# Performance work log

Measured on AMD Instinct MI355X. Metric: run time of the kernel, lower is better.

The kernel has to match this reference:

```python
import jax, jax.numpy as jnp
import numpy as np

HIDDEN = 4096
NUM_HEADS = 32
NUM_KV_HEADS = 8
HEAD_DIM = 128


def setup_inputs() -> dict:
    key = jax.random.key(0)
    k0, k1, k2, k3, k4 = jax.random.split(key, 5)
    B, S = 1, 2048
    s = 0.02
    return {
        "hidden_states": jax.random.normal(k0, (B, S, HIDDEN), dtype=jnp.float32),
        "Wq": jax.random.normal(k1, (HIDDEN, NUM_HEADS * HEAD_DIM), dtype=jnp.float32) * s,
        "Wk": jax.random.normal(k2, (HIDDEN, NUM_KV_HEADS * HEAD_DIM), dtype=jnp.float32) * s,
        "Wv": jax.random.normal(k3, (HIDDEN, NUM_KV_HEADS * HEAD_DIM), dtype=jnp.float32) * s,
        "Wo": jax.random.normal(k4, (NUM_HEADS * HEAD_DIM, HIDDEN), dtype=jnp.float32) * s,
    }


def reference(hidden_states, Wq, Wk, Wv, Wo):
    B, S, _ = hidden_states.shape
    n_rep = NUM_HEADS // NUM_KV_HEADS
    # Projections -> [B, H, S, D]
    q = (hidden_states @ Wq).reshape(B, S, NUM_HEADS, HEAD_DIM).transpose(0, 2, 1, 3)
    k = (hidden_states @ Wk).reshape(B, S, NUM_KV_HEADS, HEAD_DIM).transpose(0, 2, 1, 3)
    v = (hidden_states @ Wv).reshape(B, S, NUM_KV_HEADS, HEAD_DIM).transpose(0, 2, 1, 3)
    # GQA expansion: repeat_interleave KV heads to match query head count
    k = jnp.repeat(k, n_rep, axis=1)
    v = jnp.repeat(v, n_rep, axis=1)
    scale = HEAD_DIM ** -0.5
    # Full [B, H, S, S] attention scores (faithful to the naive reference)
    scores = jnp.einsum("bhqd,bhkd->bhqk", q, k) * scale
    causal = jnp.tril(jnp.ones((S, S), dtype=bool))
    scores = jnp.where(causal[None, None], scores, jnp.float32(-jnp.inf))
    probs = jax.nn.softmax(scores, axis=-1)
    out = jnp.einsum("bhqk,bhkd->bhqd", probs, v)
    out = out.transpose(0, 2, 1, 3).reshape(B, S, NUM_HEADS * HEAD_DIM)
    return out @ Wo
```

## Files before the change

kernel.cpp:

```cpp
#include <hip/hip_runtime.h>
#include <hip/hip_bf16.h>

typedef __bf16 bf16;
typedef __bf16 bf16x4 __attribute__((ext_vector_type(4)));
typedef __bf16 bf16x8 __attribute__((ext_vector_type(8)));
typedef float  f32x4  __attribute__((ext_vector_type(4)));

#define SEQ  2048
#define HID  4096
#define QKVN 6144

__device__ __forceinline__ void gload_lds16(const void* g, void* l) {
  __builtin_amdgcn_global_load_lds(
      (const __attribute__((address_space(1))) void*)g,
      (__attribute__((address_space(3))) void*)l, 16, 0, 0);
}

__global__ __launch_bounds__(256) void cast_f32_bf16(const float* __restrict__ in,
                                                     bf16* __restrict__ out, int n) {
  int i = (blockIdx.x * 256 + threadIdx.x) * 4;
  int stride = gridDim.x * 256 * 4;
  for (; i < n; i += stride) {
    float4 v = *(const float4*)(in + i);
    bf16x4 o;
    o[0] = (bf16)v.x; o[1] = (bf16)v.y; o[2] = (bf16)v.z; o[3] = (bf16)v.w;
    *(bf16x4*)(out + i) = o;
  }
}

__global__ __launch_bounds__(256) void transpose_cast(const float* __restrict__ W,
                                                      bf16* __restrict__ Wt,
                                                      int N, int roff) {
  __shared__ float tile[32][33];
  int k0 = blockIdx.y * 32;
  int n0 = blockIdx.x * 32;
  int t = threadIdx.x;
  int r = t >> 5, c = t & 31;
#pragma unroll
  for (int p = 0; p < 4; ++p)
    tile[r + p * 8][c] = W[(size_t)(k0 + r + p * 8) * N + n0 + c];
  __syncthreads();
#pragma unroll
  for (int p = 0; p < 4; ++p)
    Wt[(size_t)(roff + n0 + r + p * 8) * 4096 + k0 + c] = (bf16)tile[c][r + p * 8];
}

__global__ __launch_bounds__(256) void transpose_v(const bf16* __restrict__ QKV,
                                                   bf16* __restrict__ Vt_g) {
  __shared__ bf16 tile[32][33];
  int s0 = blockIdx.x * 32;
  int d0 = blockIdx.y * 32;
  int g  = blockIdx.z;
  int t = threadIdx.x;
  int r = t >> 5, c = t & 31;
#pragma unroll
  for (int p = 0; p < 4; ++p)
    tile[r + p * 8][c] = QKV[(size_t)(s0 + r + p * 8) * QKVN + 5120 + g * 128 + d0 + c];
  __syncthreads();
#pragma unroll
  for (int p = 0; p < 4; ++p)
    Vt_g[(size_t)(g * 128 + d0 + r + p * 8) * SEQ + s0 + c] = tile[c][r + p * 8];
}

template <typename OUT_T>
__global__ __launch_bounds__(256) void gemm_bt(const bf16* __restrict__ A,
                                               const bf16* __restrict__ Bt,
                                               OUT_T* __restrict__ C,
                                               int K, int ldc) {
  __shared__ __align__(16) bf16 Abuf[128 * 32];
  __shared__ __align__(16) bf16 Bbuf[128 * 32];
  int m0 = blockIdx.y * 128, n0 = blockIdx.x * 128;
  int tid = threadIdx.x, w = tid >> 6, lane = tid & 63;
  int wr = w >> 1, wc = w & 1;
  int l15 = lane & 15, l4 = lane >> 4;
  f32x4 acc[4][4] = {};
  const int nk = K >> 5;
  for (int kt = 0; kt < nk; ++kt) {
    int k0 = kt << 5;
#pragma unroll
    for (int p = 0; p < 2; ++p) {
      int elem = p * 2048 + w * 512 + lane * 8;
      int row = elem >> 5, col = elem & 31;
      gload_lds16(A + (size_t)(m0 + row) * K + k0 + col, (char*)Abuf + 2 * elem);
      gload_lds16(Bt + (size_t)(n0 + row) * K + k0 + col, (char*)Bbuf + 2 * elem);
    }
    __syncthreads();
    bf16x8 af[4], bfr[4];
#pragma unroll
    for (int m = 0; m < 4; ++m)
      af[m] = *(const bf16x8*)(Abuf + (wr * 64 + m * 16 + l15) * 32 + l4 * 8);
#pragma unroll
    for (int n = 0; n < 4; ++n)
      bfr[n] = *(const bf16x8*)(Bbuf + (wc * 64 + n * 16 + l15) * 32 + l4 * 8);
#pragma unroll
    for (int m = 0; m < 4; ++m)
#pragma unroll
      for (int n = 0; n < 4; ++n)
        acc[m][n] = __builtin_amdgcn_mfma_f32_16x16x32_bf16(af[m], bfr[n], acc[m][n], 0, 0, 0);
    __syncthreads();
  }
#pragma unroll
  for (int m = 0; m < 4; ++m)
#pragma unroll
    for (int n = 0; n < 4; ++n)
#pragma unroll
      for (int i = 0; i < 4; ++i) {
        int row = m0 + wr * 64 + m * 16 + l4 * 4 + i;
        int col = n0 + wc * 64 + n * 16 + l15;
        C[(size_t)row * ldc + col] = (OUT_T)acc[m][n][i];
      }
}

__global__ __launch_bounds__(512, 2) void attn_kernel(const bf16* __restrict__ QKV,
                                                      const bf16* __restrict__ Vt_g,
                                                      bf16* __restrict__ attn) {
  __shared__ __align__(16) bf16 Klds[2][64 * 128];
  __shared__ __align__(16) bf16 Vlds[2][64 * 128];
  __shared__ __align__(16) bf16 Plds[8 * 16 * 64];
  const int bid = blockIdx.x;
  const int g = bid & 7;
  const int rest = bid >> 3;
  const int hg = rest & 1;
  const int pair = rest >> 1;
  const int qb_a = pair, qb_b = 31 - pair;
  const int tid = threadIdx.x, w = tid >> 6, lane = tid & 63;
  const int hsel = w >> 2, qw = w & 3;
  const int h = g * 4 + hg * 2 + hsel;
  const int l15 = lane & 15, l4 = lane >> 4;
  const int wqA = qb_a * 64 + qw * 16;
  const int wqB = qb_b * 64 + qw * 16;
  const int qcol = h * 128;
  const int kcol = 4096 + g * 128;
  const float scale = 0.08838834764831845f;
  const float LOG2E = 1.4426950408889634f;

  const bf16* Vhead = Vt_g + (size_t)g * 128 * SEQ;

  bf16x8 aqA[4], aqB[4];
#pragma unroll
  for (int kc = 0; kc < 4; ++kc) {
    aqA[kc] = *(const bf16x8*)(QKV + (size_t)(wqA + l15) * QKVN + qcol + kc * 32 + l4 * 8);
    aqB[kc] = *(const bf16x8*)(QKV + (size_t)(wqB + l15) * QKVN + qcol + kc * 32 + l4 * 8);
  }

  f32x4 acc_oA[8] = {}, acc_oB[8] = {};
  float mA[4], lA[4], mB[4], lB[4];
#pragma unroll
  for (int i = 0; i < 4; ++i) { mA[i] = -1e30f; lA[i] = 0.f; mB[i] = -1e30f; lB[i] = 0.f; }

  auto stageKV = [&](int kb, int buf) {
#pragma unroll
    for (int j = 0; j < 2; ++j) {
      int c = tid + (j << 9);
      int krow = c >> 4, kslot = c & 15;
      gload_lds16((const char*)(QKV + (size_t)(kb + krow) * QKVN + kcol) +
                      ((kslot ^ (krow & 7)) << 4),
                  (char*)Klds[buf] + c * 16);
      int vrow = c >> 3, vslot = c & 7;
      gload_lds16(Vhead + (size_t)vrow * SEQ + kb + ((vslot ^ (vrow & 7)) << 3),
                  (char*)Vlds[buf] + c * 16);
    }
  };

  auto compute_block = [&](const bf16x8* aq, f32x4* acc_o, float* mrow, float* lrow,
                           int wq0, int kb, int cur) {
    const char* Kbuf = (const char*)Klds[cur];
    const char* Vbuf = (const char*)Vlds[cur];
    f32x4 accs[4] = {};
#pragma unroll
    for (int n = 0; n < 4; ++n) {
      int row_ = n * 16 + l15;
      int sw = (row_ & 7) << 4;
#pragma unroll
      for (int kc = 0; kc < 4; ++kc) {
        bf16x8 bk = *(const bf16x8*)(Kbuf + row_ * 256 + ((kc * 64 + l4 * 16) ^ sw));
        accs[n] = __builtin_amdgcn_mfma_f32_16x16x32_bf16(aq[kc], bk, accs[n], 0, 0, 0);
      }
    }
    bool needmask = (kb + 64 > wq0);
    float s[4][4];
#pragma unroll
    for (int n = 0; n < 4; ++n)
#pragma unroll
      for (int i = 0; i < 4; ++i) {
        float v = accs[n][i] * scale;
        if (needmask) {
          int ks = kb + n * 16 + l15;
          int qr = wq0 + l4 * 4 + i;
          if (ks > qr) v = -1e30f;
        }
        s[n][i] = v;
      }
    float fac[4], ps[4][4];
#pragma unroll
    for (int i = 0; i < 4; ++i) {
      float t = fmaxf(fmaxf(s[0][i], s[1][i]), fmaxf(s[2][i], s[3][i]));
      t = fmaxf(t, __shfl_xor(t, 1));
      t = fmaxf(t, __shfl_xor(t, 2));
      t = fmaxf(t, __shfl_xor(t, 4));
      t = fmaxf(t, __shfl_xor(t, 8));
      float mnew = fmaxf(mrow[i], t);
      fac[i] = exp2f((mrow[i] - mnew) * LOG2E);
      float psum = 0.f;
#pragma unroll
      for (int n = 0; n < 4; ++n) {
        float p = exp2f((s[n][i] - mnew) * LOG2E);
        ps[n][i] = p; psum += p;
      }
      psum += __shfl_xor(psum, 1);
      psum += __shfl_xor(psum, 2);
      psum += __shfl_xor(psum, 4);
      psum += __shfl_xor(psum, 8);
      lrow[i] = lrow[i] * fac[i] + psum;
      mrow[i] = mnew;
    }
#pragma unroll
    for (int n2 = 0; n2 < 8; ++n2)
#pragma unroll
      for (int i = 0; i < 4; ++i)
        acc_o[n2][i] *= fac[i];
    char* Pw = (char*)Plds + w * 2048;
#pragma unroll
    for (int n = 0; n < 4; ++n)
#pragma unroll
      for (int i = 0; i < 4; ++i) {
        int r = l4 * 4 + i;
        int b = (r * 128 + (n * 16 + l15) * 2) ^ ((r & 7) << 4);
        *(bf16*)(Pw + b) = (bf16)ps[n][i];
      }
    __builtin_amdgcn_sched_barrier(0);
    asm volatile("" ::: "memory");
    bf16x8 pa[2];
#pragma unroll
    for (int kc = 0; kc < 2; ++kc)
      pa[kc] = *(const bf16x8*)(Pw + (l15 * 128 + ((kc * 64 + l4 * 16) ^ ((l15 & 7) << 4))));
#pragma unroll
    for (int n2 = 0; n2 < 8; ++n2) {
      int row_ = n2 * 16 + l15;
      int sw = (row_ & 7) << 4;
#pragma unroll
      for (int kc = 0; kc < 2; ++kc) {
        bf16x8 bv = *(const bf16x8*)(Vbuf + row_ * 128 + ((kc * 64 + l4 * 16) ^ sw));
        acc_o[n2] = __builtin_amdgcn_mfma_f32_16x16x32_bf16(pa[kc], bv, acc_o[n2], 0, 0, 0);
      }
    }
    asm volatile("" ::: "memory");
  };

  stageKV(0, 0);
  __syncthreads();

  int cur = 0;
  for (int kbi = 0; kbi <= qb_b; ++kbi) {
    int kb = kbi * 64;
    if (kbi < qb_b) stageKV(kb + 64, cur ^ 1);
    if (kbi <= qb_a) compute_block(aqA, acc_oA, mA, lA, wqA, kb, cur);
    compute_block(aqB, acc_oB, mB, lB, wqB, kb, cur);
    __syncthreads();
    cur ^= 1;
  }

#pragma unroll
  for (int n2 = 0; n2 < 8; ++n2)
#pragma unroll
    for (int i = 0; i < 4; ++i) {
      int col = qcol + n2 * 16 + l15;
      attn[(size_t)(wqA + l4 * 4 + i) * 4096 + col] = (bf16)(acc_oA[n2][i] / lA[i]);
      attn[(size_t)(wqB + l4 * 4 + i) * 4096 + col] = (bf16)(acc_oB[n2][i] / lB[i]);
    }
}

extern "C" void kernel_launch(void* const* d_in, const int* in_sizes, int n_in,
                              void* d_out, int out_size, void* d_ws, size_t ws_size,
                              hipStream_t stream) {
  const float* X  = (const float*)d_in[0];
  const float* Wq = (const float*)d_in[1];
  const float* Wk = (const float*)d_in[2];
  const float* Wv = (const float*)d_in[3];
  const float* Wo = (const float*)d_in[4];
  float* out = (float*)d_out;

  const size_t XB_OFF  = 0;
  const size_t WT_OFF  = 16777216;
  const size_t VT_OFF  = WT_OFF + 33554432;
  const size_t QKV_OFF = 16777216 + 50331648;
  if (ws_size < (size_t)92274688) return;

  char* ws = (char*)d_ws;
  bf16* Xb    = (bf16*)(ws + XB_OFF);
  bf16* Wt    = (bf16*)(ws + WT_OFF);
  bf16* Vt_g  = (bf16*)(ws + VT_OFF);
  bf16* QKV   = (bf16*)(ws + QKV_OFF);
  bf16* attnb = Xb;

  cast_f32_bf16<<<2048, 256, 0, stream>>>(X, Xb, SEQ * HID);
  transpose_cast<<<dim3(4096 / 32, 4096 / 32), 256, 0, stream>>>(Wq, Wt, 4096, 0);
  transpose_cast<<<dim3(1024 / 32, 4096 / 32), 256, 0, stream>>>(Wk, Wt, 1024, 4096);
  transpose_cast<<<dim3(1024 / 32, 4096 / 32), 256, 0, stream>>>(Wv, Wt, 1024, 5120);
  gemm_bt<bf16><<<dim3(QKVN / 128, SEQ / 128), 256, 0, stream>>>(Xb, Wt, QKV, HID, QKVN);
  transpose_cast<<<dim3(4096 / 32, 4096 / 32), 256, 0, stream>>>(Wo, Wt, 4096, 0);
  transpose_v<<<dim3(SEQ / 32, 4, 8), 256, 0, stream>>>(QKV, Vt_g);
  attn_kernel<<<256, 512, 0, stream>>>(QKV, Vt_g, attnb);
  gemm_bt<float><<<dim3(4096 / 128, SEQ / 128), 256, 0, stream>>>(attnb, Wt, out, HID, 4096);
}
```

Before: 413.9 us.

## Deepen GEMM K-tile with swizzled LDS, add lazy softmax rescale and MFMA priority

The GEMM K-tile per iteration grows from 32 to 64, using an XOR-swizzled LDS layout to avoid bank conflicts and halving the number of barriers per K. The attention kernel skips the online-softmax rescale of the accumulators unless some row's max has grown by more than a threshold, following the FA4 lazy-rescale trick. It also raises wave priority around the MFMA sections with s_setprio. Lazy rescaling lets probabilities exceed 1 (up to about e^8) before normalization, which is fine in fp32 but relies on the bf16 P values staying in range. The larger tiles double GEMM LDS use.

```diff
diff --git a/kernel.cpp b/kernel.cpp
--- a/kernel.cpp
+++ b/kernel.cpp
@@ -67,36 +67,50 @@
                                                const bf16* __restrict__ Bt,
                                                OUT_T* __restrict__ C,
                                                int K, int ldc) {
-  __shared__ __align__(16) bf16 Abuf[128 * 32];
-  __shared__ __align__(16) bf16 Bbuf[128 * 32];
+  __shared__ __align__(16) bf16 Abuf[128 * 64];
+  __shared__ __align__(16) bf16 Bbuf[128 * 64];
   int m0 = blockIdx.y * 128, n0 = blockIdx.x * 128;
   int tid = threadIdx.x, w = tid >> 6, lane = tid & 63;
   int wr = w >> 1, wc = w & 1;
   int l15 = lane & 15, l4 = lane >> 4;
   f32x4 acc[4][4] = {};
-  const int nk = K >> 5;
+  const int nk = K >> 6;
   for (int kt = 0; kt < nk; ++kt) {
-    int k0 = kt << 5;
-#pragma unroll
-    for (int p = 0; p < 2; ++p) {
-      int elem = p * 2048 + w * 512 + lane * 8;
-      int row = elem >> 5, col = elem & 31;
-      gload_lds16(A + (size_t)(m0 + row) * K + k0 + col, (char*)Abuf + 2 * elem);
-      gload_lds16(Bt + (size_t)(n0 + row) * K + k0 + col, (char*)Bbuf + 2 * elem);
+    int k0 = kt << 6;
+#pragma unroll
+    for (int p = 0; p < 4; ++p) {
+      int c = p * 256 + tid;
+      int row = c >> 3, slot = c & 7;
+      int ssl = (slot ^ (row & 7)) << 4;
+      gload_lds16((const char*)(A + (size_t)(m0 + row) * K + k0) + ssl, (char*)Abuf + c * 16);
+      gload_lds16((const char*)(Bt + (size_t)(n0 + row) * K + k0) + ssl, (char*)Bbuf + c * 16);
     }
     __syncthreads();
-    bf16x8 af[4], bfr[4];
+    bf16x8 af[4][2], bfr[4][2];
 #pragma unroll
     for (int m = 0; m < 4; ++m)
-      af[m] = *(const bf16x8*)(Abuf + (wr * 64 + m * 16 + l15) * 32 + l4 * 8);
+#pragma unroll
+      for (int kk = 0; kk < 2; ++kk) {
+        int row = wr * 64 + m * 16 + l15;
+        af[m][kk] = *(const bf16x8*)((const char*)Abuf + row * 128 +
+                                     (((kk * 4 + l4) ^ (row & 7)) << 4));
+      }
 #pragma unroll
     for (int n = 0; n < 4; ++n)
-      bfr[n] = *(const bf16x8*)(Bbuf + (wc * 64 + n * 16 + l15) * 32 + l4 * 8);
-#pragma unroll
-    for (int m = 0; m < 4; ++m)
-#pragma unroll
-      for (int n = 0; n < 4; ++n)
-        acc[m][n] = __builtin_amdgcn_mfma_f32_16x16x32_bf16(af[m], bfr[n], acc[m][n], 0, 0, 0);
+#pragma unroll
+      for (int kk = 0; kk < 2; ++kk) {
+        int row = wc * 64 + n * 16 + l15;
+        bfr[n][kk] = *(const bf16x8*)((const char*)Bbuf + row * 128 +
+                                      (((kk * 4 + l4) ^ (row & 7)) << 4));
+      }
+#pragma unroll
+    for (int kk = 0; kk < 2; ++kk)
+#pragma unroll
+      for (int m = 0; m < 4; ++m)
+#pragma unroll
+        for (int n = 0; n < 4; ++n)
+          acc[m][n] = __builtin_amdgcn_mfma_f32_16x16x32_bf16(af[m][kk], bfr[n][kk],
+                                                              acc[m][n], 0, 0, 0);
     __syncthreads();
   }
 #pragma unroll
@@ -167,6 +181,7 @@
     const char* Kbuf = (const char*)Klds[cur];
     const char* Vbuf = (const char*)Vlds[cur];
     f32x4 accs[4] = {};
+    __builtin_amdgcn_s_setprio(1);
 #pragma unroll
     for (int n = 0; n < 4; ++n) {
       int row_ = n * 16 + l15;
@@ -177,6 +192,7 @@
         accs[n] = __builtin_amdgcn_mfma_f32_16x16x32_bf16(aq[kc], bk, accs[n], 0, 0, 0);
       }
     }
+    __builtin_amdgcn_s_setprio(0);
     bool needmask = (kb + 64 > wq0);
     float s[4][4];
 #pragma unroll
@@ -191,7 +207,7 @@
         }
         s[n][i] = v;
       }
-    float fac[4], ps[4][4];
+    float t4[4];
 #pragma unroll
     for (int i = 0; i < 4; ++i) {
       float t = fmaxf(fmaxf(s[0][i], s[1][i]), fmaxf(s[2][i], s[3][i]));
@@ -199,26 +215,40 @@
       t = fmaxf(t, __shfl_xor(t, 2));
       t = fmaxf(t, __shfl_xor(t, 4));
       t = fmaxf(t, __shfl_xor(t, 8));
-      float mnew = fmaxf(mrow[i], t);
-      fac[i] = exp2f((mrow[i] - mnew) * LOG2E);
+      t4[i] = t;
+    }
+    float dm = fmaxf(fmaxf(t4[0] - mrow[0], t4[1] - mrow[1]),
+                     fmaxf(t4[2] - mrow[2], t4[3] - mrow[3]));
+    if (!__all(dm <= 8.0f)) {
+      float fac[4];
+#pragma unroll
+      for (int i = 0; i < 4; ++i) {
+        float mnew = fmaxf(mrow[i], t4[i]);
+        fac[i] = exp2f((mrow[i] - mnew) * LOG2E);
+        mrow[i] = mnew;
+        lrow[i] *= fac[i];
+      }
+#pragma unroll
+      for (int n2 = 0; n2 < 8; ++n2)
+#pragma unroll
+        for (int i = 0; i < 4; ++i)
+          acc_o[n2][i] *= fac[i];
+    }
+    float ps[4][4];
+#pragma unroll
+    for (int i = 0; i < 4; ++i) {
       float psum = 0.f;
 #pragma unroll
       for (int n = 0; n < 4; ++n) {
-        float p = exp2f((s[n][i] - mnew) * LOG2E);
+        float p = exp2f((s[n][i] - mrow[i]) * LOG2E);
         ps[n][i] = p; psum += p;
       }
       psum += __shfl_xor(psum, 1);
       psum += __shfl_xor(psum, 2);
       psum += __shfl_xor(psum, 4);
       psum += __shfl_xor(psum, 8);
-      lrow[i] = lrow[i] * fac[i] + psum;
-      mrow[i] = mnew;
-    }
-#pragma unroll
-    for (int n2 = 0; n2 < 8; ++n2)
-#pragma unroll
-      for (int i = 0; i < 4; ++i)
-        acc_o[n2][i] *= fac[i];
+      lrow[i] += psum;
+    }
     char* Pw = (char*)Plds + w * 2048;
 #pragma unroll
     for (int n = 0; n < 4; ++n)
@@ -234,6 +264,7 @@
 #pragma unroll
     for (int kc = 0; kc < 2; ++kc)
       pa[kc] = *(const bf16x8*)(Pw + (l15 * 128 + ((kc * 64 + l4 * 16) ^ ((l15 & 7) << 4))));
+    __builtin_amdgcn_s_setprio(1);
 #pragma unroll
     for (int n2 = 0; n2 < 8; ++n2) {
       int row_ = n2 * 16 + l15;
@@ -244,6 +275,7 @@
         acc_o[n2] = __builtin_amdgcn_mfma_f32_16x16x32_bf16(pa[kc], bv, acc_o[n2], 0, 0, 0);
       }
     }
+    __builtin_amdgcn_s_setprio(0);
     asm volatile("" ::: "memory");
   };
 
```

New measurement: 379.0 us. 8.4% less time.
